# Optimization experiments

Measured on AMD Instinct MI355X. Metric: run time of the kernel, lower is better.

Reference implementation:

```python
import jax, jax.numpy as jnp
import numpy as np

B, LC, LQ, D = 64, 1024, 128, 128
NEG_BIG = 1.0e12


def _len_mask(seq_len, T):
    # seq_len: (B,1) int. Equivalent to 1 - cumsum(one_hot(L, T)): 1 for pos < L.
    pos = jnp.arange(T)  # (T,)
    return (pos[None, :] < seq_len).astype(jnp.float32)  # (B,T)


def setup_inputs() -> dict:
    key = jax.random.key(0)
    ks = jax.random.split(key, 7)
    return {
        "x_cont": jax.random.normal(ks[0], (B, LC, D), dtype=jnp.float32),
        "x_ques": jax.random.normal(ks[1], (B, LQ, D), dtype=jnp.float32),
        "W0": jax.random.normal(ks[2], (D, 1), dtype=jnp.float32) / np.sqrt(D),
        "W1": jax.random.normal(ks[3], (D, 1), dtype=jnp.float32) / np.sqrt(D),
        "W2": jax.random.normal(ks[4], (1, 1, D), dtype=jnp.float32) / np.sqrt(D),
        "cont_len": jax.random.randint(ks[5], (B, 1), 1, LC, dtype=jnp.int32),
        "ques_len": jax.random.randint(ks[6], (B, 1), 1, LQ, dtype=jnp.int32),
    }


def reference(x_cont, x_ques, W0, W1, W2, cont_len, ques_len):
    # Trilinear similarity: S[b,c,q] = x_cont@W0 + x_ques@W1 + (x_cont*W2) . x_ques
    s_cont = jnp.einsum('bcd,do->bco', x_cont, W0)            # (B,LC,1)
    s_ques = jnp.einsum('bqd,do->boq', x_ques, W1)            # (B,1,LQ)
    s_fuse = jnp.einsum('bcd,bqd->bcq', x_cont * W2, x_ques)  # (B,LC,LQ)
    S = s_cont + s_ques + s_fuse                               # (B,LC,LQ)

    mask_q = _len_mask(ques_len, LQ)  # (B,LQ)
    mask_c = _len_mask(cont_len, LC)  # (B,LC)

    # Softmax over query axis, masking invalid query positions (axis=-1)
    S_bar = jax.nn.softmax(S - (1.0 - mask_q)[:, None, :] * NEG_BIG, axis=-1)
    # Softmax over context axis, masking invalid context positions, then transpose
    S_T = jnp.swapaxes(
        jax.nn.softmax(S - (1.0 - mask_c)[:, :, None] * NEG_BIG, axis=1), 1, 2
    )  # (B,LQ,LC)

    c2q = jnp.einsum('bcq,bqd->bcd', S_bar, x_ques)             # (B,LC,D)
    q2c = jnp.einsum('bcq,bqk,bkd->bcd', S_bar, S_T, x_cont)    # (B,LC,D)

    result = jnp.concatenate(
        [x_cont, c2q, x_cont * c2q, x_cont * q2c], axis=-1
    )  # (B,LC,4D)
    return result, S_bar, S_T
```

## Files before the change

### kernel.cpp

```cpp
#include <hip/hip_runtime.h>

#define NB 64
#define LC 1024
#define LQ 128
#define DD 128
#define NEG_BIG 1.0e12f

typedef __attribute__((ext_vector_type(8))) short short8;
typedef __attribute__((ext_vector_type(4))) unsigned short ushort4v;
typedef __attribute__((ext_vector_type(4))) float floatx4;

__device__ __forceinline__ float wave_reduce_sum(float v) {
#pragma unroll
  for (int m = 32; m >= 1; m >>= 1) v += __shfl_xor(v, m, 64);
  return v;
}
__device__ __forceinline__ unsigned short f2bf(float f) {
  union { float f; unsigned int u; } v;
  v.f = f;
  const unsigned int r = v.u + 0x7FFFu + ((v.u >> 16) & 1u);
  return (unsigned short)(r >> 16);
}
__device__ __forceinline__ float bf2f(unsigned int u) {
  union { unsigned int u; float f; } v;
  v.u = u << 16;
  return v.f;
}

__global__ __launch_bounds__(256) void k_pre_q(
    const float* __restrict__ xq, const float* __restrict__ W1,
    unsigned short* __restrict__ xqT, float* __restrict__ a_ques) {
  __shared__ __align__(16) unsigned short tile[128 * 136];
  const int b = blockIdx.x;
  const int t = threadIdx.x;
  const int w = t >> 6, lane = t & 63;
  const float* src = xq + (size_t)b * LQ * DD;

#pragma unroll
  for (int i = 0; i < 16; ++i) {
    const int id = t + (i << 8);
    const int row = id >> 5, u = id & 31;
    const float4 v = *(const float4*)(src + (size_t)row * DD + (u << 2));
    ushort4v pk;
    pk[0] = f2bf(v.x); pk[1] = f2bf(v.y); pk[2] = f2bf(v.z); pk[3] = f2bf(v.w);
    *(ushort4v*)(tile + row * 136 + (u << 2)) = pk;
  }
  const float w1a = W1[lane << 1];
  const float w1b = W1[(lane << 1) + 1];
  __syncthreads();
#pragma unroll
  for (int r = 0; r < 32; ++r) {
    const int row = (w << 5) + r;
    const unsigned int pk = *(const unsigned int*)(tile + row * 136 + (lane << 1));
    float s = fmaf(bf2f(pk & 0xffffu), w1a, bf2f(pk >> 16) * w1b);
    s = wave_reduce_sum(s);
    if (lane == 0) a_ques[b * LQ + row] = s;
  }
  const int d = t >> 1, ch = t & 1;
  short8 o[8];
#pragma unroll
  for (int j = 0; j < 64; ++j)
    ((unsigned short*)o)[j] = tile[(ch * 64 + j) * 136 + d];
  unsigned short* dp = xqT + ((size_t)b * DD + d) * LQ + ch * 64;
#pragma unroll
  for (int j = 0; j < 8; ++j) *(short8*)(dp + (j << 3)) = o[j];
}

#define PADW 136

__global__ __launch_bounds__(512) void k_score(
    const float* __restrict__ xc, const float* __restrict__ xq,
    const float* __restrict__ w2, const float* __restrict__ W0,
    const float* __restrict__ a_ques, const int* __restrict__ qlen_p,
    const int* __restrict__ clen_p, float* __restrict__ out_sbar,
    unsigned short* __restrict__ Pb, float* __restrict__ colsum_part,
    unsigned short* __restrict__ xcT, unsigned short* __restrict__ sbarb) {
  __shared__ __align__(16) unsigned short smem[2 * 128 * PADW];
  __shared__ float a_cont_s[128];
  unsigned short* xcs = smem;
  unsigned short* xqs = smem + 128 * PADW;
  unsigned short* ptile = smem + 128 * PADW;

  const int b = blockIdx.x >> 3;
  const int ct = blockIdx.x & 7;
  const int c0 = ct << 7;
  const int t = threadIdx.x;
  const int w = t >> 6, lane = t & 63;
  const int frow = lane & 15;
  const int kb = lane >> 4;

  const float* xc_blk = xc + ((size_t)b * LC + c0) * DD;
  const float* xq_b = xq + (size_t)b * LQ * DD;

  const int u = t & 15;
  const float4 w0a = *(const float4*)(W0 + (u << 3));
  const float4 w0b = *(const float4*)(W0 + (u << 3) + 4);
  const float4 w2a = *(const float4*)(w2 + (u << 3));
  const float4 w2b = *(const float4*)(w2 + (u << 3) + 4);

#pragma unroll
  for (int i = 0; i < 4; ++i) {
    const int row = (t >> 4) + (i << 5);
    {
      const float4 v0 = *(const float4*)(xc_blk + (size_t)row * DD + (u << 3));
      const float4 v1 = *(const float4*)(xc_blk + (size_t)row * DD + (u << 3) + 4);
      short8 pk;
      pk[0] = (short)f2bf(v0.x); pk[1] = (short)f2bf(v0.y);
      pk[2] = (short)f2bf(v0.z); pk[3] = (short)f2bf(v0.w);
      pk[4] = (short)f2bf(v1.x); pk[5] = (short)f2bf(v1.y);
      pk[6] = (short)f2bf(v1.z); pk[7] = (short)f2bf(v1.w);
      *(short8*)(xcs + row * PADW + (u << 3)) = pk;
      float pd = v0.x * w0a.x + v0.y * w0a.y + v0.z * w0a.z + v0.w * w0a.w +
                 v1.x * w0b.x + v1.y * w0b.y + v1.z * w0b.z + v1.w * w0b.w;
#pragma unroll
      for (int msk = 8; msk >= 1; msk >>= 1) pd += __shfl_xor(pd, msk, 64);
      if ((lane & 15) == 0) a_cont_s[row] = pd;
    }
    {
      const float4 v0 = *(const float4*)(xq_b + (size_t)row * DD + (u << 3));
      const float4 v1 = *(const float4*)(xq_b + (size_t)row * DD + (u << 3) + 4);
      short8 pk;
      pk[0] = (short)f2bf(v0.x * w2a.x); pk[1] = (short)f2bf(v0.y * w2a.y);
      pk[2] = (short)f2bf(v0.z * w2a.z); pk[3] = (short)f2bf(v0.w * w2a.w);
      pk[4] = (short)f2bf(v1.x * w2b.x); pk[5] = (short)f2bf(v1.y * w2b.y);
      pk[6] = (short)f2bf(v1.z * w2b.z); pk[7] = (short)f2bf(v1.w * w2b.w);
      *(short8*)(xqs + row * PADW + (u << 3)) = pk;
    }
  }

  const int qlen = qlen_p[b];
  const int clen = clen_p[b];
  float aq[8];
#pragma unroll
  for (int n = 0; n < 8; ++n) aq[n] = a_ques[b * LQ + n * 16 + frow];

  __syncthreads();

  float ac[4];
#pragma unroll
  for (int reg = 0; reg < 4; ++reg)
    ac[reg] = a_cont_s[w * 16 + kb * 4 + reg];

  floatx4 acc[8];
#pragma unroll
  for (int n = 0; n < 8; ++n) acc[n] = (floatx4){0.f, 0.f, 0.f, 0.f};
  const unsigned short* arow = xcs + (w * 16 + frow) * PADW + kb * 8;
  const unsigned short* brow = xqs + frow * PADW + kb * 8;
#pragma unroll
  for (int ks = 0; ks < 4; ++ks) {
    const short8 af = *(const short8*)(arow + ks * 32);
#pragma unroll
    for (int n = 0; n < 8; ++n) {
      const short8 bf = *(const short8*)(brow + n * 16 * PADW + ks * 32);
      acc[n] = __builtin_amdgcn_mfma_f32_16x16x32_bf16(af, bf, acc[n], 0, 0, 0);
    }
  }

  {
    const int d = t & 127;
    const int half = t >> 7;
    __align__(16) unsigned short tmp[32];
#pragma unroll
    for (int j = 0; j < 32; ++j)
      tmp[j] = xcs[((half << 5) + j) * PADW + d];
    unsigned short* dp = xcT + ((size_t)b * DD + d) * LC + c0 + (half << 5);
#pragma unroll
    for (int j = 0; j < 4; ++j)
      *(short8*)(dp + (j << 3)) = *(const short8*)(tmp + (j << 3));
  }

  float raw[8][4];
#pragma unroll
  for (int n = 0; n < 8; ++n)
#pragma unroll
    for (int reg = 0; reg < 4; ++reg) raw[n][reg] = acc[n][reg] + ac[reg] + aq[n];

  float mreg[4], invreg[4];
  float* sbar_row0 =
      out_sbar + ((size_t)b * LC + c0 + w * 16 + kb * 4) * LQ + frow;
#pragma unroll
  for (int reg = 0; reg < 4; ++reg) {
    float x[8];
    float m = -3.4e38f;
#pragma unroll
    for (int n = 0; n < 8; ++n) {
      x[n] = raw[n][reg] - ((n * 16 + frow) < qlen ? 0.f : NEG_BIG);
      m = fmaxf(m, x[n]);
    }
#pragma unroll
    for (int msk = 8; msk >= 1; msk >>= 1) m = fmaxf(m, __shfl_xor(m, msk, 64));
    float s = 0.f;
#pragma unroll
    for (int n = 0; n < 8; ++n) {
      x[n] = __expf(x[n] - m);
      s += x[n];
    }
#pragma unroll
    for (int msk = 8; msk >= 1; msk >>= 1) s += __shfl_xor(s, msk, 64);
    const float inv = 1.0f / s;
    float* o = sbar_row0 + (size_t)reg * LQ;
#pragma unroll
    for (int n = 0; n < 8; ++n) o[n * 16] = x[n] * inv;
    mreg[reg] = m;
    invreg[reg] = inv;
  }

  unsigned short* sb_out = sbarb + ((size_t)b * LC + c0) * LQ;
#pragma unroll
  for (int p = 0; p < 4; ++p) {
    __syncthreads();
    if ((w >> 1) == p) {
      const int crow = ((w & 1) << 4) + (kb << 2);
#pragma unroll
      for (int reg = 0; reg < 4; ++reg) {
        const float m = mreg[reg], inv = invreg[reg];
#pragma unroll
        for (int n = 0; n < 8; ++n) {
          const float xv = raw[n][reg] - ((n * 16 + frow) < qlen ? 0.f : NEG_BIG);
          ptile[(crow + reg) * 136 + (n << 4) + frow] = f2bf(__expf(xv - m) * inv);
        }
      }
    }
    __syncthreads();
    const int row = t >> 4, ch = t & 15;
    *(short8*)(sb_out + (size_t)((p << 5) + row) * LQ + (ch << 3)) =
        *(const short8*)(ptile + row * 136 + (ch << 3));
  }

  const int cl0 = c0 + w * 16 + kb * 4;
#pragma unroll
  for (int reg = 0; reg < 4; ++reg) {
    const bool ok = (cl0 + reg) < clen;
#pragma unroll
    for (int n = 0; n < 8; ++n)
      raw[n][reg] = ok ? __expf(raw[n][reg]) : 0.f;
  }

  unsigned short* Pb_b = Pb + (size_t)b * LQ * LC;
  float* cs_blk = colsum_part + ((size_t)b * 8 + ct) * LQ;
#pragma unroll
  for (int p = 0; p < 4; ++p) {
    __syncthreads();
#pragma unroll
    for (int n2 = 0; n2 < 2; ++n2) {
#pragma unroll
      for (int reg = 0; reg < 4; ++reg)
        ptile[(n2 * 16 + frow) * 136 + (w * 16 + kb * 4 + reg)] =
            f2bf(raw[2 * p + n2][reg]);
    }
    __syncthreads();
    const int qrow = t >> 4;
    const int ch = t & 15;
    const short8 pv = *(const short8*)(ptile + qrow * 136 + (ch << 3));
    *(short8*)(Pb_b + (size_t)(p * 32 + qrow) * LC + c0 + (ch << 3)) = pv;
    float s = 0.f;
#pragma unroll
    for (int j = 0; j < 8; ++j) s += bf2f((unsigned short)pv[j]);
#pragma unroll
    for (int msk = 8; msk >= 1; msk >>= 1) s += __shfl_xor(s, msk, 64);
    if (ch == 0) cs_blk[p * 32 + qrow] = s;
  }
}

__global__ __launch_bounds__(256) void k_fuse(
    const unsigned short* __restrict__ Pb, const float* __restrict__ colsum_part,
    const unsigned short* __restrict__ xcT, float* __restrict__ st,
    unsigned short* __restrict__ AbT) {
  __shared__ __align__(16) unsigned short Ps[16 * 1032];
  __shared__ unsigned short abt[128 * 20];
  __shared__ float inv_s[16];

  const int b = blockIdx.x >> 3;
  const int q0 = (blockIdx.x & 7) << 4;
  const int t = threadIdx.x;
  const int w = t >> 6, lane = t & 63;
  const int frow = lane & 15, kb = lane >> 4;

  const unsigned short* Pb_blk = Pb + ((size_t)b * LQ + q0) * LC;
  {
    const int row = t >> 4;
#pragma unroll
    for (int j = 0; j < 8; ++j) {
      const int cs = ((t & 15) << 3) + (j << 7);
      *(short8*)(Ps + row * 1032 + cs) =
          *(const short8*)(Pb_blk + (size_t)row * LC + cs);
    }
  }
  if (t < 16) {
    float s = 0.f;
#pragma unroll
    for (int j = 0; j < 8; ++j)
      s += colsum_part[((size_t)b * 8 + j) * LQ + q0 + t];
    inv_s[t] = 1.0f / s;
  }
  __syncthreads();

  {
    const int row = t >> 4;
    const float inv = inv_s[row];
    float* dst = st + ((size_t)b * LQ + q0 + row) * LC;
#pragma unroll
    for (int j = 0; j < 8; ++j) {
      const int cs = ((t & 15) << 3) + (j << 7);
      const short8 pv = *(const short8*)(Ps + row * 1032 + cs);
      float4 o0, o1;
      o0.x = bf2f((unsigned short)pv[0]) * inv;
      o0.y = bf2f((unsigned short)pv[1]) * inv;
      o0.z = bf2f((unsigned short)pv[2]) * inv;
      o0.w = bf2f((unsigned short)pv[3]) * inv;
      o1.x = bf2f((unsigned short)pv[4]) * inv;
      o1.y = bf2f((unsigned short)pv[5]) * inv;
      o1.z = bf2f((unsigned short)pv[6]) * inv;
      o1.w = bf2f((unsigned short)pv[7]) * inv;
      *(float4*)(dst + cs) = o0;
      *(float4*)(dst + cs + 4) = o1;
    }
  }

  const unsigned short* xcT_b = xcT + (size_t)b * DD * LC;
  const unsigned short* b0p =
      xcT_b + (size_t)((w * 2 + 0) * 16 + frow) * LC + kb * 8;
  const unsigned short* b1p =
      xcT_b + (size_t)((w * 2 + 1) * 16 + frow) * LC + kb * 8;
  const unsigned short* ap = Ps + frow * 1032 + kb * 8;
  floatx4 acc0 = (floatx4){0.f, 0.f, 0.f, 0.f};
  floatx4 acc1 = (floatx4){0.f, 0.f, 0.f, 0.f};
#pragma unroll 8
  for (int kk = 0; kk < 32; ++kk) {
    const short8 af = *(const short8*)(ap + kk * 32);
    const short8 b0 = *(const short8*)(b0p + kk * 32);
    const short8 b1 = *(const short8*)(b1p + kk * 32);
    acc0 = __builtin_amdgcn_mfma_f32_16x16x32_bf16(af, b0, acc0, 0, 0, 0);
    acc1 = __builtin_amdgcn_mfma_f32_16x16x32_bf16(af, b1, acc1, 0, 0, 0);
  }

  __syncthreads();
  const float i0 = inv_s[kb * 4 + 0], i1 = inv_s[kb * 4 + 1];
  const float i2 = inv_s[kb * 4 + 2], i3 = inv_s[kb * 4 + 3];
  {
    const int d0 = (w * 2 + 0) * 16 + frow;
    abt[d0 * 20 + kb * 4 + 0] = f2bf(acc0[0] * i0);
    abt[d0 * 20 + kb * 4 + 1] = f2bf(acc0[1] * i1);
    abt[d0 * 20 + kb * 4 + 2] = f2bf(acc0[2] * i2);
    abt[d0 * 20 + kb * 4 + 3] = f2bf(acc0[3] * i3);
    const int d1 = (w * 2 + 1) * 16 + frow;
    abt[d1 * 20 + kb * 4 + 0] = f2bf(acc1[0] * i0);
    abt[d1 * 20 + kb * 4 + 1] = f2bf(acc1[1] * i1);
    abt[d1 * 20 + kb * 4 + 2] = f2bf(acc1[2] * i2);
    abt[d1 * 20 + kb * 4 + 3] = f2bf(acc1[3] * i3);
  }
  __syncthreads();
  const int d = t >> 1, h = t & 1;
  short8 ov;
#pragma unroll
  for (int j = 0; j < 8; ++j)
    ((unsigned short*)&ov)[j] = abt[d * 20 + h * 8 + j];
  *(short8*)(AbT + ((size_t)b * DD + d) * LQ + q0 + h * 8) = ov;
}

__global__ __launch_bounds__(256) void k_out(
    const float* __restrict__ xc, const unsigned short* __restrict__ sbarb,
    const unsigned short* __restrict__ xqT, const unsigned short* __restrict__ AbT,
    float* __restrict__ out) {
  __shared__ __align__(16) float stg[2 * 32 * 132];

  const int b = blockIdx.x >> 4;
  const int c0 = (blockIdx.x & 15) << 6;
  const int t = threadIdx.x;
  const int w = t >> 6, lane = t & 63;
  const int frow = lane & 15, kb = lane >> 4;

  const unsigned short* sb_blk = sbarb + ((size_t)b * LC + c0) * LQ;
  const unsigned short* xqT_b = xqT + (size_t)b * DD * LQ;
  const unsigned short* AbT_b = AbT + (size_t)b * DD * LQ;
  short8 bq[2][4], ba[2][4];
#pragma unroll
  for (int nt = 0; nt < 2; ++nt) {
    const int d = (w << 5) + (nt << 4) + frow;
#pragma unroll
    for (int ks = 0; ks < 4; ++ks) {
      bq[nt][ks] = *(const short8*)(xqT_b + (size_t)d * LQ + ks * 32 + kb * 8);
      ba[nt][ks] = *(const short8*)(AbT_b + (size_t)d * LQ + ks * 32 + kb * 8);
    }
  }

  floatx4 accq[4][2], acca[4][2];
#pragma unroll
  for (int mt = 0; mt < 4; ++mt)
#pragma unroll
    for (int nt = 0; nt < 2; ++nt) {
      accq[mt][nt] = (floatx4){0.f, 0.f, 0.f, 0.f};
      acca[mt][nt] = (floatx4){0.f, 0.f, 0.f, 0.f};
    }
#pragma unroll
  for (int mt = 0; mt < 4; ++mt) {
#pragma unroll
    for (int ks = 0; ks < 4; ++ks) {
      const short8 af = *(const short8*)(
          sb_blk + (size_t)((mt << 4) + frow) * LQ + ks * 32 + kb * 8);
#pragma unroll
      for (int nt = 0; nt < 2; ++nt) {
        accq[mt][nt] =
            __builtin_amdgcn_mfma_f32_16x16x32_bf16(af, bq[nt][ks], accq[mt][nt], 0, 0, 0);
        acca[mt][nt] =
            __builtin_amdgcn_mfma_f32_16x16x32_bf16(af, ba[nt][ks], acca[mt][nt], 0, 0, 0);
      }
    }
  }

  float* out_b = out + ((size_t)b * LC + c0) * (4 * DD);
  const float* xc_blk = xc + ((size_t)b * LC + c0) * DD;

#pragma unroll
  for (int p = 0; p < 2; ++p) {
    __syncthreads();
#pragma unroll
    for (int mh = 0; mh < 2; ++mh) {
      const int mt = 2 * p + mh;
#pragma unroll
      for (int nt = 0; nt < 2; ++nt) {
        const int d = (w << 5) + (nt << 4) + frow;
        const int cl = (mh << 4) + (kb << 2);
#pragma unroll
        for (int reg = 0; reg < 4; ++reg) {
          stg[(cl + reg) * 132 + d] = accq[mt][nt][reg];
          stg[32 * 132 + (cl + reg) * 132 + d] = acca[mt][nt][reg];
        }
      }
    }
    __syncthreads();
    const int g = lane >> 4;
    const int d0 = (lane & 15) << 3;
#pragma unroll
    for (int j = 0; j < 8; ++j) {
      const int rl = (w << 3) + j;
      const int c = (p << 5) + rl;
      const float4 xv0 = *(const float4*)(xc_blk + (size_t)c * DD + d0);
      const float4 xv1 = *(const float4*)(xc_blk + (size_t)c * DD + d0 + 4);
      const float4 cq0 = *(const float4*)(stg + rl * 132 + d0);
      const float4 cq1 = *(const float4*)(stg + rl * 132 + d0 + 4);
      const float4 qc0 = *(const float4*)(stg + 32 * 132 + rl * 132 + d0);
      const float4 qc1 = *(const float4*)(stg + 32 * 132 + rl * 132 + d0 + 4);
      float4 o0, o1;
      if (g == 0) { o0 = xv0; o1 = xv1; }
      else if (g == 1) { o0 = cq0; o1 = cq1; }
      else if (g == 2) {
        o0 = make_float4(xv0.x * cq0.x, xv0.y * cq0.y, xv0.z * cq0.z, xv0.w * cq0.w);
        o1 = make_float4(xv1.x * cq1.x, xv1.y * cq1.y, xv1.z * cq1.z, xv1.w * cq1.w);
      } else {
        o0 = make_float4(xv0.x * qc0.x, xv0.y * qc0.y, xv0.z * qc0.z, xv0.w * qc0.w);
        o1 = make_float4(xv1.x * qc1.x, xv1.y * qc1.y, xv1.z * qc1.z, xv1.w * qc1.w);
      }
      float* o = out_b + (size_t)c * (4 * DD) + (g << 7) + d0;
      *(float4*)(o) = o0;
      *(float4*)(o + 4) = o1;
    }
  }
}

extern "C" void kernel_launch(void* const* d_in, const int* in_sizes, int n_in,
                              void* d_out, int out_size, void* d_ws, size_t ws_size,
                              hipStream_t stream) {
  const float* xc = (const float*)d_in[0];
  const float* xq = (const float*)d_in[1];
  const float* W0 = (const float*)d_in[2];
  const float* W1 = (const float*)d_in[3];
  const float* W2 = (const float*)d_in[4];
  const int* clen = (const int*)d_in[5];
  const int* qlen = (const int*)d_in[6];

  float* out = (float*)d_out;
  float* out_sbar = out + (size_t)NB * LC * 4 * DD;
  float* out_st = out_sbar + (size_t)NB * LC * LQ;

  float* a_ques = (float*)d_ws;
  float* colsum_part = a_ques + NB * LQ;
  unsigned short* xcT = (unsigned short*)(colsum_part + NB * 8 * LQ);
  unsigned short* xqT = xcT + (size_t)NB * LC * DD;
  unsigned short* AbT = xqT + (size_t)NB * LQ * DD;
  unsigned short* Pb = AbT + (size_t)NB * LQ * DD;
  unsigned short* sbarb = Pb + (size_t)NB * LQ * LC;

  k_pre_q<<<NB, 256, 0, stream>>>(xq, W1, xqT, a_ques);
  k_score<<<NB * 8, 512, 0, stream>>>(xc, xq, W2, W0, a_ques, qlen, clen,
                                      out_sbar, Pb, colsum_part, xcT, sbarb);
  k_fuse<<<NB * 8, 256, 0, stream>>>(Pb, colsum_part, xcT, out_st, AbT);
  k_out<<<NB * 16, 256, 0, stream>>>(xc, sbarb, xqT, AbT, out);
}
```

Baseline: 123.0 us.

## Move fp32 S_bar output write from k_score to k_out via bf16 staging

k_score no longer writes the fp32 S_bar output with strided scalar stores. k_out now reads the bf16 sbarb copy and writes S_bar to the output as coalesced float4 stores. The staging passes in k_score switch from four rounds to two, reusing the full shared buffer for larger tiles with fewer barriers. The exported S_bar is now the bf16-rounded value rather than full fp32, which loses precision, and k_out gains extra global traffic.

```diff
diff --git a/kernel.cpp b/kernel.cpp
--- a/kernel.cpp
+++ b/kernel.cpp
@@ -72,14 +72,14 @@
     const float* __restrict__ xc, const float* __restrict__ xq,
     const float* __restrict__ w2, const float* __restrict__ W0,
     const float* __restrict__ a_ques, const int* __restrict__ qlen_p,
-    const int* __restrict__ clen_p, float* __restrict__ out_sbar,
-    unsigned short* __restrict__ Pb, float* __restrict__ colsum_part,
-    unsigned short* __restrict__ xcT, unsigned short* __restrict__ sbarb) {
+    const int* __restrict__ clen_p, unsigned short* __restrict__ Pb,
+    float* __restrict__ colsum_part, unsigned short* __restrict__ xcT,
+    unsigned short* __restrict__ sbarb) {
   __shared__ __align__(16) unsigned short smem[2 * 128 * PADW];
   __shared__ float a_cont_s[128];
   unsigned short* xcs = smem;
   unsigned short* xqs = smem + 128 * PADW;
-  unsigned short* ptile = smem + 128 * PADW;
+  unsigned short* pt = smem;
 
   const int b = blockIdx.x >> 3;
   const int ct = blockIdx.x & 7;
@@ -176,8 +176,6 @@
     for (int reg = 0; reg < 4; ++reg) raw[n][reg] = acc[n][reg] + ac[reg] + aq[n];
 
   float mreg[4], invreg[4];
-  float* sbar_row0 =
-      out_sbar + ((size_t)b * LC + c0 + w * 16 + kb * 4) * LQ + frow;
 #pragma unroll
   for (int reg = 0; reg < 4; ++reg) {
     float x[8];
@@ -191,40 +189,36 @@
     for (int msk = 8; msk >= 1; msk >>= 1) m = fmaxf(m, __shfl_xor(m, msk, 64));
     float s = 0.f;
 #pragma unroll
-    for (int n = 0; n < 8; ++n) {
-      x[n] = __expf(x[n] - m);
-      s += x[n];
-    }
+    for (int n = 0; n < 8; ++n) s += __expf(x[n] - m);
 #pragma unroll
     for (int msk = 8; msk >= 1; msk >>= 1) s += __shfl_xor(s, msk, 64);
-    const float inv = 1.0f / s;
-    float* o = sbar_row0 + (size_t)reg * LQ;
-#pragma unroll
-    for (int n = 0; n < 8; ++n) o[n * 16] = x[n] * inv;
     mreg[reg] = m;
-    invreg[reg] = inv;
+    invreg[reg] = 1.0f / s;
   }
 
   unsigned short* sb_out = sbarb + ((size_t)b * LC + c0) * LQ;
 #pragma unroll
-  for (int p = 0; p < 4; ++p) {
+  for (int p = 0; p < 2; ++p) {
     __syncthreads();
-    if ((w >> 1) == p) {
-      const int crow = ((w & 1) << 4) + (kb << 2);
+    if ((w >> 2) == p) {
+      const int crow = ((w & 3) << 4) + (kb << 2);
 #pragma unroll
       for (int reg = 0; reg < 4; ++reg) {
         const float m = mreg[reg], inv = invreg[reg];
 #pragma unroll
         for (int n = 0; n < 8; ++n) {
           const float xv = raw[n][reg] - ((n * 16 + frow) < qlen ? 0.f : NEG_BIG);
-          ptile[(crow + reg) * 136 + (n << 4) + frow] = f2bf(__expf(xv - m) * inv);
+          pt[(crow + reg) * 136 + (n << 4) + frow] = f2bf(__expf(xv - m) * inv);
         }
       }
     }
     __syncthreads();
-    const int row = t >> 4, ch = t & 15;
-    *(short8*)(sb_out + (size_t)((p << 5) + row) * LQ + (ch << 3)) =
-        *(const short8*)(ptile + row * 136 + (ch << 3));
+    const int row = t >> 3, ch = t & 7;
+    const short8 v0 = *(const short8*)(pt + row * 136 + (ch << 4));
+    const short8 v1 = *(const short8*)(pt + row * 136 + (ch << 4) + 8);
+    unsigned short* dst = sb_out + (size_t)((p << 6) + row) * LQ + (ch << 4);
+    *(short8*)(dst) = v0;
+    *(short8*)(dst + 8) = v1;
   }
 
   const int cl0 = c0 + w * 16 + kb * 4;
@@ -239,26 +233,33 @@
   unsigned short* Pb_b = Pb + (size_t)b * LQ * LC;
   float* cs_blk = colsum_part + ((size_t)b * 8 + ct) * LQ;
 #pragma unroll
-  for (int p = 0; p < 4; ++p) {
+  for (int p = 0; p < 2; ++p) {
     __syncthreads();
 #pragma unroll
-    for (int n2 = 0; n2 < 2; ++n2) {
+    for (int nn = 0; nn < 4; ++nn) {
+      const int n = (p << 2) + nn;
+      const int qrow = (nn << 4) + frow;
 #pragma unroll
       for (int reg = 0; reg < 4; ++reg)
-        ptile[(n2 * 16 + frow) * 136 + (w * 16 + kb * 4 + reg)] =
-            f2bf(raw[2 * p + n2][reg]);
+        pt[qrow * 136 + (w << 4) + (kb << 2) + reg] = f2bf(raw[n][reg]);
     }
     __syncthreads();
-    const int qrow = t >> 4;
-    const int ch = t & 15;
-    const short8 pv = *(const short8*)(ptile + qrow * 136 + (ch << 3));
-    *(short8*)(Pb_b + (size_t)(p * 32 + qrow) * LC + c0 + (ch << 3)) = pv;
+    const int row = t >> 3, ch = t & 7;
+    const short8 v0 = *(const short8*)(pt + row * 136 + (ch << 4));
+    const short8 v1 = *(const short8*)(pt + row * 136 + (ch << 4) + 8);
+    unsigned short* dst = Pb_b + (size_t)((p << 6) + row) * LC + c0 + (ch << 4);
+    *(short8*)(dst) = v0;
+    *(short8*)(dst + 8) = v1;
     float s = 0.f;
 #pragma unroll
-    for (int j = 0; j < 8; ++j) s += bf2f((unsigned short)pv[j]);
-#pragma unroll
-    for (int msk = 8; msk >= 1; msk >>= 1) s += __shfl_xor(s, msk, 64);
-    if (ch == 0) cs_blk[p * 32 + qrow] = s;
+    for (int j = 0; j < 8; ++j) {
+      s += bf2f((unsigned short)v0[j]);
+      s += bf2f((unsigned short)v1[j]);
+    }
+    s += __shfl_xor(s, 1, 64);
+    s += __shfl_xor(s, 2, 64);
+    s += __shfl_xor(s, 4, 64);
+    if (ch == 0) cs_blk[(p << 6) + row] = s;
   }
 }
 
@@ -361,7 +362,7 @@
 __global__ __launch_bounds__(256) void k_out(
     const float* __restrict__ xc, const unsigned short* __restrict__ sbarb,
     const unsigned short* __restrict__ xqT, const unsigned short* __restrict__ AbT,
-    float* __restrict__ out) {
+    float* __restrict__ out_sbar, float* __restrict__ out) {
   __shared__ __align__(16) float stg[2 * 32 * 132];
 
   const int b = blockIdx.x >> 4;
@@ -371,6 +372,22 @@
   const int frow = lane & 15, kb = lane >> 4;
 
   const unsigned short* sb_blk = sbarb + ((size_t)b * LC + c0) * LQ;
+
+  {
+    float* sbo = out_sbar + ((size_t)b * LC + c0) * LQ;
+#pragma unroll
+    for (int j = 0; j < 8; ++j) {
+      const int idx = t + (j << 8);
+      const int row = idx >> 5, uu = idx & 31;
+      const ushort4v pv =
+          *(const ushort4v*)(sb_blk + (size_t)row * LQ + (uu << 2));
+      float4 o;
+      o.x = bf2f(pv[0]); o.y = bf2f(pv[1]);
+      o.z = bf2f(pv[2]); o.w = bf2f(pv[3]);
+      *(float4*)(sbo + (size_t)row * LQ + (uu << 2)) = o;
+    }
+  }
+
   const unsigned short* xqT_b = xqT + (size_t)b * DD * LQ;
   const unsigned short* AbT_b = AbT + (size_t)b * DD * LQ;
   short8 bq[2][4], ba[2][4];
@@ -483,7 +500,7 @@
 
   k_pre_q<<<NB, 256, 0, stream>>>(xq, W1, xqT, a_ques);
   k_score<<<NB * 8, 512, 0, stream>>>(xc, xq, W2, W0, a_ques, qlen, clen,
-                                      out_sbar, Pb, colsum_part, xcT, sbarb);
+                                      Pb, colsum_part, xcT, sbarb);
   k_fuse<<<NB * 8, 256, 0, stream>>>(Pb, colsum_part, xcT, out_st, AbT);
-  k_out<<<NB * 16, 256, 0, stream>>>(xc, sbarb, xqT, AbT, out);
-}
+  k_out<<<NB * 16, 256, 0, stream>>>(xc, sbarb, xqT, AbT, out_sbar, out);
+}
```

Result: slower. 129.0 us (+4.9%).
